# Performance work log

Hardware: AMD Instinct MI355X
Metric: run time of the kernel (lower is better)

The kernel has to match this reference:

```python
import jax, jax.numpy as jnp
import numpy as np
from jax import lax

H, W = 32, 32
HEADS = 8
EPS_LN = 1e-5


def layer_norm(x, g, b):
    mu = jnp.mean(x, axis=-1, keepdims=True)
    var = jnp.mean((x - mu) ** 2, axis=-1, keepdims=True)
    return (x - mu) * lax.rsqrt(var + EPS_LN) * g + b


def l2norm(x):  # F.normalize along last dim, eps=1e-12
    n = jnp.sqrt(jnp.sum(x * x, axis=-1, keepdims=True))
    return x / jnp.maximum(n, 1e-12)


def channel_attention(x, qkv_w, temp, proj_w, proj_b):
    B, N, C = x.shape
    d = C // HEADS
    qkv = (x @ qkv_w).reshape(B, N, 3, HEADS, d).transpose(2, 0, 3, 1, 4)  # [3,B,h,N,d]
    q, k, v = qkv[0], qkv[1], qkv[2]
    q = l2norm(q.swapaxes(-2, -1))  # [B,h,d,N], normalized over N
    k = l2norm(k.swapaxes(-2, -1))
    v = v.swapaxes(-2, -1)          # [B,h,d,N]
    attn = jnp.einsum('bhdn,bhen->bhde', q, k) * temp  # [B,h,d,d]
    attn = jax.nn.softmax(attn, axis=-1)
    out = jnp.einsum('bhde,bhen->bhdn', attn, v)       # [B,h,d,N]
    out = out.transpose(0, 3, 1, 2).reshape(B, N, C)
    return out @ proj_w + proj_b


def cross_attention(x1, x2, rp_w, rp_b, cn_g, cn_b):
    # head_count = 1 (efficient/linear attention)
    B, N, D = x1.shape
    keys = x2.swapaxes(1, 2)            # [B,D,N]
    values = x1.swapaxes(1, 2)          # [B,D,N]
    key = jax.nn.softmax(keys, axis=2)  # softmax over tokens
    query = jax.nn.softmax(keys, axis=1)  # softmax over channels
    context = jnp.einsum('bdn,ben->bde', key, values)     # [B,Dk,Dv]
    attended = jnp.einsum('bde,bdn->ben', context, query)  # [B,Dv,N]
    agg = attended.reshape(B, D, H, W)
    # 1x1 conv reprojection D -> 2D
    rep = jnp.einsum('bdhw,ed->behw', agg, rp_w) + rp_b[None, :, None, None]
    rep = rep.reshape(B, 2 * D, N).transpose(0, 2, 1)     # [B,N,2D]
    return layer_norm(rep, cn_g, cn_b)


def mix_ffn(x, fc1_w, fc1_b, dw_w, dw_b, fc2_w, fc2_b):
    B, N, _ = x.shape
    c2 = fc1_w.shape[1]
    h1 = x @ fc1_w + fc1_b                                 # [B,N,c2]
    t = h1.swapaxes(1, 2).reshape(B, c2, H, W)
    conv = lax.conv_general_dilated(
        t, dw_w, window_strides=(1, 1), padding='SAME',
        feature_group_count=c2,
        dimension_numbers=('NCHW', 'OIHW', 'NCHW')) + dw_b[None, :, None, None]
    h2 = conv.reshape(B, c2, N).swapaxes(1, 2)             # [B,N,c2]
    return jax.nn.gelu(h2, approximate=False) @ fc2_w + fc2_b


def reference(x1, x2, ln1_g, ln1_b, ca_qkv_w, ca_temp, ca_proj_w, ca_proj_b,
              ln3_g, ln3_b, rp_w, rp_b, cn_g, cn_b, ln2_g, ln2_b,
              fc1_w, fc1_b, dw_w, dw_b, fc2_w, fc2_b):
    # NOTE: original code uses norm1 + channel_attn1 on BOTH streams
    channel1 = x1 + channel_attention(layer_norm(x1, ln1_g, ln1_b), ca_qkv_w, ca_temp, ca_proj_w, ca_proj_b)
    channel2 = x2 + channel_attention(layer_norm(x2, ln1_g, ln1_b), ca_qkv_w, ca_temp, ca_proj_w, ca_proj_b)
    n1 = layer_norm(channel1, ln3_g, ln3_b)
    n2 = layer_norm(channel2, ln3_g, ln3_b)
    attn = cross_attention(n1, n2, rp_w, rp_b, cn_g, cn_b)
    tx = jnp.concatenate([channel1, channel2], axis=2) + attn  # [B,N,2D]
    mx = tx + mix_ffn(layer_norm(tx, ln2_g, ln2_b), fc1_w, fc1_b, dw_w, dw_b, fc2_w, fc2_b)
    return mx


def setup_inputs() -> dict:
    key = jax.random.key(0)
    ks = jax.random.split(key, 8)
    B, N, D = 16, 1024, 384
    s = 0.02
    return {
        'x1': jax.random.normal(ks[0], (B, N, D), jnp.float32),
        'x2': jax.random.normal(ks[1], (B, N, D), jnp.float32),
        'ln1_g': jnp.ones((D,), jnp.float32), 'ln1_b': jnp.zeros((D,), jnp.float32),
        'ca_qkv_w': jax.random.normal(ks[2], (D, 3 * D), jnp.float32) * s,
        'ca_temp': jnp.ones((HEADS, 1, 1), jnp.float32),
        'ca_proj_w': jax.random.normal(ks[3], (D, D), jnp.float32) * s,
        'ca_proj_b': jnp.zeros((D,), jnp.float32),
        'ln3_g': jnp.ones((D,), jnp.float32), 'ln3_b': jnp.zeros((D,), jnp.float32),
        'rp_w': jax.random.normal(ks[4], (2 * D, D), jnp.float32) * s,
        'rp_b': jnp.zeros((2 * D,), jnp.float32),
        'cn_g': jnp.ones((2 * D,), jnp.float32), 'cn_b': jnp.zeros((2 * D,), jnp.float32),
        'ln2_g': jnp.ones((2 * D,), jnp.float32), 'ln2_b': jnp.zeros((2 * D,), jnp.float32),
        'fc1_w': jax.random.normal(ks[5], (2 * D, 4 * D), jnp.float32) * s,
        'fc1_b': jnp.zeros((4 * D,), jnp.float32),
        'dw_w': jax.random.normal(ks[6], (4 * D, 1, 3, 3), jnp.float32) * s,
        'dw_b': jnp.zeros((4 * D,), jnp.float32),
        'fc2_w': jax.random.normal(ks[7], (4 * D, 2 * D), jnp.float32) * s,
        'fc2_b': jnp.zeros((2 * D,), jnp.float32),
    }
```

## Files before the change

kernel.cpp:

```cpp
#include <hip/hip_runtime.h>
#include <math.h>

#define BN 16
#define NN 1024
#define DD 384
#define D2 768
#define C2 1536
#define NHEAD 8
#define DH 48

#define SZ_ND   (BN*NN*DD)
#define SZ_N2D  (BN*NN*D2)
#define SZ_NC2  (BN*NN*C2)
#define M2      32768
#define MH      16384

typedef __bf16 bf16x8 __attribute__((ext_vector_type(8)));
typedef float f32x4v __attribute__((ext_vector_type(4)));
typedef unsigned short u16x4 __attribute__((ext_vector_type(4)));

__device__ __forceinline__ unsigned short f2bf(float x){
  unsigned int u = __float_as_uint(x);
  u += 0x7FFFu + ((u >> 16) & 1u);
  return (unsigned short)(u >> 16);
}
__device__ __forceinline__ float bf2f(unsigned short h){
  return __uint_as_float(((unsigned int)h) << 16);
}

__device__ __forceinline__ float blockReduceSum256(float v){
  __shared__ float red[4];
  #pragma unroll
  for (int o=32;o;o>>=1) v += __shfl_down(v,o,64);
  if ((threadIdx.x&63)==0) red[threadIdx.x>>6]=v;
  __syncthreads();
  float r = red[0]+red[1]+red[2]+red[3];
  __syncthreads();
  return r;
}
__device__ __forceinline__ float blockReduceMax256(float v){
  __shared__ float red[4];
  #pragma unroll
  for (int o=32;o;o>>=1) v = fmaxf(v, __shfl_down(v,o,64));
  if ((threadIdx.x&63)==0) red[threadIdx.x>>6]=v;
  __syncthreads();
  float r = fmaxf(fmaxf(red[0],red[1]),fmaxf(red[2],red[3]));
  __syncthreads();
  return r;
}

__global__ __launch_bounds__(256) void ln_kernel(const float* __restrict__ in,
    const float* __restrict__ g, const float* __restrict__ b,
    float* __restrict__ out, int C){
  const int row = blockIdx.x;
  const float* x = in + (size_t)row*C;
  float s=0.f;
  for (int i=threadIdx.x;i<C;i+=256) s += x[i];
  s = blockReduceSum256(s);
  const float mu = s / (float)C;
  float v=0.f;
  for (int i=threadIdx.x;i<C;i+=256){ float d = x[i]-mu; v += d*d; }
  v = blockReduceSum256(v);
  const float rs = rsqrtf(v/(float)C + 1e-5f);
  float* o = out + (size_t)row*C;
  for (int i=threadIdx.x;i<C;i+=256) o[i] = (x[i]-mu)*rs*g[i] + b[i];
}

__global__ __launch_bounds__(256) void ln_split2_kernel(const float* __restrict__ in1,
    const float* __restrict__ in2, int Mh,
    const float* __restrict__ g, const float* __restrict__ b,
    unsigned short* __restrict__ oh, unsigned short* __restrict__ ol, int C){
  const int row = blockIdx.x;
  const float* x = (row < Mh) ? (in1 + (size_t)row*C) : (in2 + (size_t)(row-Mh)*C);
  float s=0.f;
  for (int i=threadIdx.x;i<C;i+=256) s += x[i];
  s = blockReduceSum256(s);
  const float mu = s / (float)C;
  float v=0.f;
  for (int i=threadIdx.x;i<C;i+=256){ float d = x[i]-mu; v += d*d; }
  v = blockReduceSum256(v);
  const float rs = rsqrtf(v/(float)C + 1e-5f);
  unsigned short* ohp = oh + (size_t)row*C;
  unsigned short* olp = ol + (size_t)row*C;
  for (int i=threadIdx.x;i<C;i+=256){
    float val = (x[i]-mu)*rs*g[i] + b[i];
    unsigned short hh = f2bf(val);
    ohp[i] = hh; olp[i] = f2bf(val - bf2f(hh));
  }
}

__global__ __launch_bounds__(256) void rowsoftmax_split_kernel(const float* __restrict__ in,
    unsigned short* __restrict__ oh, unsigned short* __restrict__ ol, int C){
  const int row = blockIdx.x;
  const float* x = in + (size_t)row*C;
  float m = -3.0e38f;
  for (int i=threadIdx.x;i<C;i+=256) m = fmaxf(m, x[i]);
  m = blockReduceMax256(m);
  float s = 0.f;
  for (int i=threadIdx.x;i<C;i+=256) s += expf(x[i]-m);
  s = blockReduceSum256(s);
  const float inv = 1.f/s;
  unsigned short* ohp = oh + (size_t)row*C;
  unsigned short* olp = ol + (size_t)row*C;
  for (int i=threadIdx.x;i<C;i+=256){
    float p = expf(x[i]-m)*inv;
    unsigned short hh = f2bf(p);
    ohp[i] = hh; olp[i] = f2bf(p - bf2f(hh));
  }
}

__global__ __launch_bounds__(256) void colsoftmax_tsplit_kernel(const float* __restrict__ in,
    unsigned short* __restrict__ oh, unsigned short* __restrict__ ol){
  const int dl = threadIdx.x & 63;
  const int nc = threadIdx.x >> 6;
  const int d  = blockIdx.x*64 + dl;
  const int b  = blockIdx.y;
  const float* p = in + (size_t)b*NN*DD + d;
  __shared__ float redm[4][64];
  __shared__ float reds[4][64];
  float m = -3.0e38f;
  for (int n=nc*256; n<nc*256+256; n++) m = fmaxf(m, p[(size_t)n*DD]);
  redm[nc][dl] = m; __syncthreads();
  m = fmaxf(fmaxf(redm[0][dl],redm[1][dl]),fmaxf(redm[2][dl],redm[3][dl]));
  float s=0.f;
  for (int n=nc*256;n<nc*256+256;n++) s += expf(p[(size_t)n*DD]-m);
  reds[nc][dl]=s; __syncthreads();
  s = reds[0][dl]+reds[1][dl]+reds[2][dl]+reds[3][dl];
  const float inv = 1.f/s;
  unsigned short* qh = oh + ((size_t)b*DD + d)*NN;
  unsigned short* ql = ol + ((size_t)b*DD + d)*NN;
  for (int n=nc*256;n<nc*256+256;n++){
    float val = expf(p[(size_t)n*DD]-m)*inv;
    unsigned short hh = f2bf(val);
    qh[n] = hh; ql[n] = f2bf(val - bf2f(hh));
  }
}

__global__ __launch_bounds__(256) void tsplit_kernel(const float* __restrict__ in,
    unsigned short* __restrict__ oh, unsigned short* __restrict__ ol, int R, int Cc){
  const size_t zb = (size_t)blockIdx.z * R * Cc;
  const float* ip = in + zb;
  unsigned short* ohp = oh + zb;
  unsigned short* olp = ol + zb;
  __shared__ float tile[32][33];
  const int c0 = blockIdx.x*32, r0 = blockIdx.y*32;
  const int j = threadIdx.x & 31, i4 = threadIdx.x >> 5;
  #pragma unroll
  for (int s=0;s<4;s++){
    int i = i4*4+s;
    tile[i][j] = ip[(size_t)(r0+i)*Cc + c0 + j];
  }
  __syncthreads();
  #pragma unroll
  for (int s=0;s<4;s++){
    int i = i4*4+s;
    float x = tile[j][i];
    unsigned short h = f2bf(x);
    ohp[(size_t)(c0+i)*R + r0 + j] = h;
    olp[(size_t)(c0+i)*R + r0 + j] = f2bf(x - bf2f(h));
  }
}

__global__ __launch_bounds__(256) void chattn_mfma_kernel(
    const unsigned int* __restrict__ qp, const float* __restrict__ temp,
    unsigned short* __restrict__ coh, unsigned short* __restrict__ col)
{
  const int bh = blockIdx.x, b = bh >> 3, h = bh & 7;
  const int t = threadIdx.x, w = t >> 6, lane = t & 63;
  const int lr = lane & 15, g = lane >> 4;

  __shared__ __align__(16) unsigned char ldsA[27648];
  unsigned short (*Qh)[72] = (unsigned short(*)[72])(ldsA);
  unsigned short (*Ql)[72] = (unsigned short(*)[72])(ldsA + 6912);
  unsigned short (*Kh)[72] = (unsigned short(*)[72])(ldsA + 13824);
  unsigned short (*Kl)[72] = (unsigned short(*)[72])(ldsA + 20736);
  unsigned short (*Vh)[72] = (unsigned short(*)[72])(ldsA);
  unsigned short (*Vl)[72] = (unsigned short(*)[72])(ldsA + 9216);
  __shared__ unsigned short Ph[48][72], Pl[48][72];
  __shared__ float S[48][49];
  __shared__ float qn[48], kn[48];

  const size_t base = (size_t)b*NN*1152 + (size_t)h*48;

  int agrp[3], apr[3], aoff[3];
  #pragma unroll
  for (int l=0;l<3;l++){
    int idx = l*256+t;
    int mo = (idx>=384) ? 1 : 0;
    int a = idx - mo*384;
    agrp[l] = a%12; apr[l] = a/12; aoff[l] = mo*384;
  }

  f32x4v acc[12];
  #pragma unroll
  for (int i=0;i<12;i++) acc[i] = (f32x4v){0.f,0.f,0.f,0.f};

  uint4 p0[3], p1[3];
  #pragma unroll
  for (int l=0;l<3;l++){
    const size_t a = base + (size_t)(apr[l]*2)*1152 + aoff[l] + agrp[l]*4;
    p0[l] = *(const uint4*)(qp + a);
    p1[l] = *(const uint4*)(qp + a + 1152);
  }

  for (int nc=0; nc<16; nc++){
    #pragma unroll
    for (int l=0;l<3;l++){
      unsigned short (*Dh)[72] = aoff[l] ? Kh : Qh;
      unsigned short (*Dl)[72] = aoff[l] ? Kl : Ql;
      const unsigned w0[4] = {p0[l].x, p0[l].y, p0[l].z, p0[l].w};
      const unsigned w1[4] = {p1[l].x, p1[l].y, p1[l].z, p1[l].w};
      #pragma unroll
      for (int c=0;c<4;c++){
        int d = agrp[l]*4+c;
        *(unsigned int*)&Dh[d][apr[l]*2] = (w0[c] & 0xffffu) | (w1[c] << 16);
        *(unsigned int*)&Dl[d][apr[l]*2] = (w0[c] >> 16)     | (w1[c] & 0xffff0000u);
      }
    }
    __syncthreads();
    if (nc < 15){
      #pragma unroll
      for (int l=0;l<3;l++){
        const size_t a = base + (size_t)((nc+1)*64 + apr[l]*2)*1152 + aoff[l] + agrp[l]*4;
        p0[l] = *(const uint4*)(qp + a);
        p1[l] = *(const uint4*)(qp + a + 1152);
      }
    }
    if (w < 3){
      #pragma unroll
      for (int ks=0;ks<2;ks++){
        bf16x8 a_h = *(const bf16x8*)&Qh[w*16+lr][ks*32+g*8];
        bf16x8 a_l = *(const bf16x8*)&Ql[w*16+lr][ks*32+g*8];
        #pragma unroll
        for (int c=0;c<3;c++){
          bf16x8 b_h = *(const bf16x8*)&Kh[c*16+lr][ks*32+g*8];
          bf16x8 b_l = *(const bf16x8*)&Kl[c*16+lr][ks*32+g*8];
          acc[c] = __builtin_amdgcn_mfma_f32_16x16x32_bf16(a_h, b_h, acc[c], 0,0,0);
          acc[c] = __builtin_amdgcn_mfma_f32_16x16x32_bf16(a_l, b_h, acc[c], 0,0,0);
          acc[c] = __builtin_amdgcn_mfma_f32_16x16x32_bf16(a_h, b_l, acc[c], 0,0,0);
        }
      }
    } else {
      #pragma unroll
      for (int ks=0;ks<2;ks++){
        #pragma unroll
        for (int c=0;c<3;c++){
          bf16x8 qh_ = *(const bf16x8*)&Qh[c*16+lr][ks*32+g*8];
          bf16x8 ql_ = *(const bf16x8*)&Ql[c*16+lr][ks*32+g*8];
          bf16x8 kh_ = *(const bf16x8*)&Kh[c*16+lr][ks*32+g*8];
          bf16x8 kl_ = *(const bf16x8*)&Kl[c*16+lr][ks*32+g*8];
          acc[c]   = __builtin_amdgcn_mfma_f32_16x16x32_bf16(qh_, qh_, acc[c],   0,0,0);
          acc[3+c] = __builtin_amdgcn_mfma_f32_16x16x32_bf16(qh_, ql_, acc[3+c], 0,0,0);
          acc[6+c] = __builtin_amdgcn_mfma_f32_16x16x32_bf16(kh_, kh_, acc[6+c], 0,0,0);
          acc[9+c] = __builtin_amdgcn_mfma_f32_16x16x32_bf16(kh_, kl_, acc[9+c], 0,0,0);
        }
      }
    }
    __syncthreads();
  }

  const float tp = temp[h];
  if (w == 3){
    if ((lane>>4) == ((lane&15)>>2)){
      int p = lane & 15, r = p & 3;
      #pragma unroll
      for (int c=0;c<3;c++){
        float q2 = fmaxf(acc[c][r]   + 2.f*acc[3+c][r], 0.f);
        float k2 = fmaxf(acc[6+c][r] + 2.f*acc[9+c][r], 0.f);
        qn[c*16+p] = fmaxf(sqrtf(q2), 1e-12f);
        kn[c*16+p] = fmaxf(sqrtf(k2), 1e-12f);
      }
    }
  }
  __syncthreads();
  if (w < 3){
    #pragma unroll
    for (int c=0;c<3;c++){
      #pragma unroll
      for (int r=0;r<4;r++){
        int i = w*16 + g*4 + r, j = c*16 + lr;
        S[i][j] = acc[c][r]*tp/(qn[i]*kn[j]);
      }
    }
  }
  __syncthreads();

  int vgrp[3], vtk[3];
  #pragma unroll
  for (int l=0;l<3;l++){ int idx=l*256+t; vtk[l]=idx/12; vgrp[l]=idx%12; }
  uint4 pv[3];
  #pragma unroll
  for (int l=0;l<3;l++){
    const size_t a = base + (size_t)vtk[l]*1152 + 768 + vgrp[l]*4;
    pv[l] = *(const uint4*)(qp + a);
  }

  if (t < 48){
    float m = -3.0e38f;
    for (int j=0;j<48;j++) m = fmaxf(m, S[t][j]);
    float s = 0.f;
    for (int j=0;j<48;j++){ float e_ = expf(S[t][j]-m); S[t][j] = e_; s += e_; }
    float inv = 1.f/s;
    for (int j=0;j<48;j++){
      float p = S[t][j]*inv;
      unsigned short hp = f2bf(p);
      Ph[t][j] = hp; Pl[t][j] = f2bf(p - bf2f(hp));
    }
    #pragma unroll
    for (int j=48;j<64;j++){ Ph[t][j]=0; Pl[t][j]=0; }
  } else {
    const u16x4 z4 = (u16x4){0,0,0,0};
    for (int idx=t-48; idx<512; idx+=208){
      int tk = idx>>3, q = idx&7;
      if (q<4) *(u16x4*)&Vh[tk][48+(q&3)*4] = z4;
      else     *(u16x4*)&Vl[tk][48+(q&3)*4] = z4;
    }
  }
  __syncthreads();

  bf16x8 pfh[3][2], pfl[3][2];
  #pragma unroll
  for (int it=0;it<3;it++)
    #pragma unroll
    for (int ks=0;ks<2;ks++){
      pfh[it][ks] = *(const bf16x8*)&Ph[it*16+lr][ks*32+g*8];
      pfl[it][ks] = *(const bf16x8*)&Pl[it*16+lr][ks*32+g*8];
    }

  for (int vc=0; vc<16; vc++){
    #pragma unroll
    for (int l=0;l<3;l++){
      const unsigned pw[4] = {pv[l].x, pv[l].y, pv[l].z, pv[l].w};
      u16x4 hv, lv;
      #pragma unroll
      for (int c=0;c<4;c++){
        hv[c] = (unsigned short)(pw[c] & 0xffffu);
        lv[c] = (unsigned short)(pw[c] >> 16);
      }
      *(u16x4*)&Vh[vtk[l]][vgrp[l]*4] = hv;
      *(u16x4*)&Vl[vtk[l]][vgrp[l]*4] = lv;
    }
    __syncthreads();
    if (vc < 15){
      #pragma unroll
      for (int l=0;l<3;l++){
        const size_t a = base + (size_t)((vc+1)*64+vtk[l])*1152 + 768 + vgrp[l]*4;
        pv[l] = *(const uint4*)(qp + a);
      }
    }
    bf16x8 vfh[2], vfl[2];
    #pragma unroll
    for (int ks=0;ks<2;ks++){
      vfh[ks] = *(const bf16x8*)&Vh[w*16+lr][ks*32+g*8];
      vfl[ks] = *(const bf16x8*)&Vl[w*16+lr][ks*32+g*8];
    }
    f32x4v o[3];
    #pragma unroll
    for (int it=0;it<3;it++) o[it] = (f32x4v){0.f,0.f,0.f,0.f};
    #pragma unroll
    for (int it=0;it<3;it++)
      #pragma unroll
      for (int ks=0;ks<2;ks++){
        o[it] = __builtin_amdgcn_mfma_f32_16x16x32_bf16(pfh[it][ks], vfh[ks], o[it], 0,0,0);
        o[it] = __builtin_amdgcn_mfma_f32_16x16x32_bf16(pfl[it][ks], vfh[ks], o[it], 0,0,0);
        o[it] = __builtin_amdgcn_mfma_f32_16x16x32_bf16(pfh[it][ks], vfl[ks], o[it], 0,0,0);
      }
    const int n = vc*64 + w*16 + lr;
    #pragma unroll
    for (int it=0;it<3;it++){
      const size_t off = ((size_t)b*NN + n)*DD + h*48 + it*16 + g*4;
      u16x4 hv, lv;
      #pragma unroll
      for (int r=0;r<4;r++){
        float x = o[it][r];
        unsigned short hh = f2bf(x);
        hv[r] = hh; lv[r] = f2bf(x - bf2f(hh));
      }
      *(u16x4*)(coh + off) = hv;
      *(u16x4*)(col + off) = lv;
    }
    __syncthreads();
  }
}

__global__ __launch_bounds__(256) void wconv_t_kernel(const float* __restrict__ in,
    unsigned short* __restrict__ oh, unsigned short* __restrict__ ol, int K, int Nin){
  __shared__ float tile[32][33];
  const int n0 = blockIdx.x*32, k0 = blockIdx.y*32;
  const int j = threadIdx.x & 31, i4 = threadIdx.x >> 5;
  #pragma unroll
  for (int s=0;s<4;s++){
    int i = i4*4+s;
    tile[i][j] = (n0 + j < Nin) ? in[(size_t)(k0+i)*Nin + n0 + j] : 0.f;
  }
  __syncthreads();
  #pragma unroll
  for (int s=0;s<4;s++){
    int i = i4*4+s;
    float x = tile[j][i];
    unsigned short h = f2bf(x);
    oh[(size_t)(n0+i)*K + k0 + j] = h;
    ol[(size_t)(n0+i)*K + k0 + j] = f2bf(x - bf2f(h));
  }
}

__global__ __launch_bounds__(256) void wconv_kernel(const float* __restrict__ in,
    unsigned short* __restrict__ oh, unsigned short* __restrict__ ol, int n){
  int i = blockIdx.x*256 + threadIdx.x;
  if (i < n){
    float x = in[i];
    unsigned short h = f2bf(x);
    oh[i] = h;
    ol[i] = f2bf(x - bf2f(h));
  }
}

template<bool BIAS_, bool RES_, bool SPLIT_, bool PACK32_>
__global__ __launch_bounds__(256) void gemm_bf16x3s_kernel(
    const unsigned short* __restrict__ Ah, const unsigned short* __restrict__ Al,
    const unsigned short* __restrict__ Bh, const unsigned short* __restrict__ Bl,
    const float* __restrict__ bias, const float* __restrict__ res,
    const float* __restrict__ res2, int Mh2,
    float* __restrict__ C, unsigned short* __restrict__ Ch, unsigned short* __restrict__ Cl,
    int M, int N, int K, size_t sAz, size_t sBz, size_t sCz)
{
  const int t = threadIdx.x;
  const int nwg = gridDim.x*gridDim.y;
  const int lin = blockIdx.y*gridDim.x + blockIdx.x;
  const int swz = ((nwg & 7)==0) ? ((lin & 7)*(nwg >> 3) + (lin >> 3)) : lin;
  const int bx = swz % gridDim.x, by = swz / gridDim.x;
  const int m0 = by*128, n0 = bx*128;
  const size_t zo = (size_t)blockIdx.z;

  __shared__ unsigned short As_h0[128][32], As_l0[128][32];
  __shared__ unsigned short Bs_h0[128][32], Bs_l0[128][32];
  __shared__ unsigned short As_h1[128][32], As_l1[128][32];
  __shared__ unsigned short Bs_h1[128][32], Bs_l1[128][32];

  const unsigned short* Ahb = Ah + zo*sAz + (size_t)m0*K;
  const unsigned short* Alb = Al + zo*sAz + (size_t)m0*K;
  const unsigned short* Bhb = Bh + zo*sBz + (size_t)n0*K;
  const unsigned short* Blb = Bl + zo*sBz + (size_t)n0*K;

  f32x4v acc[4][4];
  #pragma unroll
  for (int i=0;i<4;i++)
    #pragma unroll
    for (int j=0;j<4;j++) acc[i][j] = (f32x4v){0.f,0.f,0.f,0.f};

  const int w  = t >> 6;
  const int wm = w >> 1, wn = w & 1;
  const int lr = t & 15, g = (t & 63) >> 4;
  const int srow = t >> 1;
  const int kb0  = (t & 1)*2;
  const int ssw  = (srow >> 1) & 3;
  const int ks0  = ((kb0+0) ^ ssw)*8;
  const int ks1  = ((kb0+1) ^ ssw)*8;

  uint4 aAh0,aAh1,aAl0,aAl1,aBh0,aBh1,aBl0,aBl1;
  uint4 bAh0,bAh1,bAl0,bAl1,bBh0,bBh1,bBl0,bBl1;

#define LOADT(P, K0) { \
    const size_t go0 = (size_t)srow*K + (size_t)(K0) + (size_t)(kb0*8); \
    P##Ah0 = *(const uint4*)(Ahb + go0); P##Ah1 = *(const uint4*)(Ahb + go0 + 8); \
    P##Al0 = *(const uint4*)(Alb + go0); P##Al1 = *(const uint4*)(Alb + go0 + 8); \
    P##Bh0 = *(const uint4*)(Bhb + go0); P##Bh1 = *(const uint4*)(Bhb + go0 + 8); \
    P##Bl0 = *(const uint4*)(Blb + go0); P##Bl1 = *(const uint4*)(Blb + go0 + 8); }

#define WRITET(BUF, P) { \
    *(uint4*)&As_h##BUF[srow][ks0] = P##Ah0; *(uint4*)&As_h##BUF[srow][ks1] = P##Ah1; \
    *(uint4*)&As_l##BUF[srow][ks0] = P##Al0; *(uint4*)&As_l##BUF[srow][ks1] = P##Al1; \
    *(uint4*)&Bs_h##BUF[srow][ks0] = P##Bh0; *(uint4*)&Bs_h##BUF[srow][ks1] = P##Bh1; \
    *(uint4*)&Bs_l##BUF[srow][ks0] = P##Bl0; *(uint4*)&Bs_l##BUF[srow][ks1] = P##Bl1; }

#define COMPUTET(BUF) { \
    bf16x8 ah[4], al[4], bhf[4], blf[4]; \
    _Pragma("unroll") \
    for (int i=0;i<4;i++){ \
      const int ra = wm*64 + i*16 + lr; \
      const int ka = (g ^ ((ra>>1)&3))*8; \
      ah[i]  = *(const bf16x8*)&As_h##BUF[ra][ka]; \
      al[i]  = *(const bf16x8*)&As_l##BUF[ra][ka]; \
      const int rb = wn*64 + i*16 + lr; \
      const int kb = (g ^ ((rb>>1)&3))*8; \
      bhf[i] = *(const bf16x8*)&Bs_h##BUF[rb][kb]; \
      blf[i] = *(const bf16x8*)&Bs_l##BUF[rb][kb]; \
    } \
    _Pragma("unroll") \
    for (int mi=0;mi<4;mi++) \
      _Pragma("unroll") \
      for (int ni=0;ni<4;ni++){ \
        f32x4v c_ = acc[mi][ni]; \
        c_ = __builtin_amdgcn_mfma_f32_16x16x32_bf16(ah[mi], bhf[ni], c_, 0,0,0); \
        c_ = __builtin_amdgcn_mfma_f32_16x16x32_bf16(al[mi], bhf[ni], c_, 0,0,0); \
        c_ = __builtin_amdgcn_mfma_f32_16x16x32_bf16(ah[mi], blf[ni], c_, 0,0,0); \
        acc[mi][ni] = c_; \
      } }

  const int nk = K >> 5;
  LOADT(a, 0);
  WRITET(0, a);
  LOADT(a, 32);
  __syncthreads();

  for (int kt = 0; kt < nk; kt += 2){
    if (kt+2 < nk) LOADT(b, (kt+2)*32);
    COMPUTET(0);
    WRITET(1, a);
    __syncthreads();
    if (kt+3 < nk) LOADT(a, (kt+3)*32);
    COMPUTET(1);
    if (kt+2 < nk){ WRITET(0, b); }
    __syncthreads();
  }

#undef LOADT
#undef WRITET
#undef COMPUTET

  if (PACK32_){
    unsigned int* Cp = (unsigned int*)Ch + zo*sCz;
    #pragma unroll
    for (int ni=0;ni<4;ni++){
      const int col = n0 + wn*64 + ni*16 + lr;
      #pragma unroll
      for (int mi=0;mi<4;mi++){
        const int r0 = m0 + wm*64 + mi*16 + g*4;
        #pragma unroll
        for (int r=0;r<4;r++){
          float v = acc[mi][ni][r];
          unsigned short hv = f2bf(v);
          unsigned short lv = f2bf(v - bf2f(hv));
          Cp[(size_t)(r0+r)*N + col] = (unsigned)hv | ((unsigned)lv << 16);
        }
      }
    }
  } else if (SPLIT_){
    unsigned short* Chb = Ch + zo*sCz;
    unsigned short* Clb = Cl + zo*sCz;
    #pragma unroll
    for (int ni=0;ni<4;ni++){
      const int col = n0 + wn*64 + ni*16 + lr;
      #pragma unroll
      for (int mi=0;mi<4;mi++){
        const int r0 = m0 + wm*64 + mi*16 + g*4;
        #pragma unroll
        for (int r=0;r<4;r++){
          float v = acc[mi][ni][r];
          unsigned short hv = f2bf(v);
          const size_t off = (size_t)(r0+r)*N + col;
          Chb[off] = hv;
          Clb[off] = f2bf(v - bf2f(hv));
        }
      }
    }
  } else {
    float* Cb = C + zo*sCz;
    const float* resb = nullptr;
    size_t roff = 0;
    if (RES_){
      if (res2 != nullptr && m0 >= Mh2){ resb = res2; roff = (size_t)Mh2; }
      else resb = res + zo*sCz;
    }
    #pragma unroll
    for (int ni=0;ni<4;ni++){
      const int col = n0 + wn*64 + ni*16 + lr;
      const float bb = BIAS_ ? bias[col] : 0.f;
      #pragma unroll
      for (int mi=0;mi<4;mi++){
        const int r0 = m0 + wm*64 + mi*16 + g*4;
        #pragma unroll
        for (int r=0;r<4;r++){
          float v = acc[mi][ni][r] + bb;
          if (RES_) v += resb[((size_t)(r0+r) - roff)*N + col];
          Cb[(size_t)(r0+r)*N + col] = v;
        }
      }
    }
  }
}

__global__ __launch_bounds__(256) void ln_concat_ln2_kernel(const float* __restrict__ rep,
    const float* __restrict__ g1, const float* __restrict__ b1,
    const float* __restrict__ ch1, const float* __restrict__ ch2,
    const float* __restrict__ g2, const float* __restrict__ b2,
    float* __restrict__ tx, unsigned short* __restrict__ y2h, unsigned short* __restrict__ y2l){
  const int row = blockIdx.x;
  const float* x = rep + (size_t)row*D2;
  float xv[3];
  float s=0.f;
  #pragma unroll
  for (int q=0;q<3;q++){ xv[q] = x[threadIdx.x + q*256]; s += xv[q]; }
  s = blockReduceSum256(s);
  const float mu = s / (float)D2;
  float v=0.f;
  #pragma unroll
  for (int q=0;q<3;q++){ float d = xv[q]-mu; v += d*d; }
  v = blockReduceSum256(v);
  const float rs = rsqrtf(v/(float)D2 + 1e-5f);
  float tv[3];
  #pragma unroll
  for (int q=0;q<3;q++){
    int i = threadIdx.x + q*256;
    float val = (xv[q]-mu)*rs*g1[i] + b1[i];
    float rv = (i<DD) ? ch1[(size_t)row*DD + i] : ch2[(size_t)row*DD + i - DD];
    tv[q] = val + rv;
    tx[(size_t)row*D2 + i] = tv[q];
  }
  float s2 = tv[0]+tv[1]+tv[2];
  s2 = blockReduceSum256(s2);
  const float mu2 = s2 / (float)D2;
  float v2=0.f;
  #pragma unroll
  for (int q=0;q<3;q++){ float d = tv[q]-mu2; v2 += d*d; }
  v2 = blockReduceSum256(v2);
  const float rs2 = rsqrtf(v2/(float)D2 + 1e-5f);
  #pragma unroll
  for (int q=0;q<3;q++){
    int i = threadIdx.x + q*256;
    float y = (tv[q]-mu2)*rs2*g2[i] + b2[i];
    unsigned short hh = f2bf(y);
    y2h[(size_t)row*D2 + i] = hh;
    y2l[(size_t)row*D2 + i] = f2bf(y - bf2f(hh));
  }
}

__global__ __launch_bounds__(256) void dwconv_gelu_kernel(const float* __restrict__ h1,
    const float* __restrict__ w, const float* __restrict__ bias,
    unsigned short* __restrict__ gh, unsigned short* __restrict__ gl){
  const int idx = blockIdx.x*256 + threadIdx.x;
  const int b   = idx / 12288;
  const int r   = idx - b*12288;
  const int hh  = r / 384;
  const int c4  = r - hh*384;
  const int c   = c4*4;
  const float* base = h1 + (size_t)b*NN*C2 + c;
  const size_t obase = ((size_t)b*NN + hh*32)*C2 + c;

  f32x4v wk[9];
  #pragma unroll
  for (int k=0;k<9;k++){
    f32x4v t_;
    #pragma unroll
    for (int q=0;q<4;q++) t_[q] = w[(size_t)(c+q)*9 + k];
    wk[k] = t_;
  }
  f32x4v bvv;
  {
    const float4 bb = *(const float4*)(bias + c);
    bvv = (f32x4v){bb.x, bb.y, bb.z, bb.w};
  }

  const bool hm = (hh > 0), hp = (hh < 31);
  const f32x4v z4 = (f32x4v){0.f,0.f,0.f,0.f};
  const size_t rm = (size_t)((hh-1)*32)*C2;
  const size_t r0 = (size_t)( hh   *32)*C2;
  const size_t rp = (size_t)((hh+1)*32)*C2;

  f32x4v A0,A1,A2, B0,B1,B2, C0,C1,C2c;
  A0=z4; A1=z4; A2=z4;
  B0 = hm ? *(const f32x4v*)(base + rm) : z4;
  B1 =      *(const f32x4v*)(base + r0);
  B2 = hp ? *(const f32x4v*)(base + rp) : z4;
  C0 = hm ? *(const f32x4v*)(base + rm + C2) : z4;
  C1 =      *(const f32x4v*)(base + r0 + C2);
  C2c= hp ? *(const f32x4v*)(base + rp + C2) : z4;

  for (int ww=0; ww<32; ww++){
    f32x4v N0,N1,N2;
    if (ww < 30){
      const size_t co_ = (size_t)(ww+2)*C2;
      N0 = hm ? *(const f32x4v*)(base + rm + co_) : z4;
      N1 =      *(const f32x4v*)(base + r0 + co_) ;
      N2 = hp ? *(const f32x4v*)(base + rp + co_) : z4;
    } else { N0=z4; N1=z4; N2=z4; }

    f32x4v s = bvv;
    s += wk[0]*A0 + wk[1]*B0 + wk[2]*C0;
    s += wk[3]*A1 + wk[4]*B1 + wk[5]*C1;
    s += wk[6]*A2 + wk[7]*B2 + wk[8]*C2c;

    u16x4 hv, lv;
    #pragma unroll
    for (int q=0;q<4;q++){
      float rlt = 0.5f*s[q]*(1.f + erff(s[q]*0.70710678118654752f));
      unsigned short hhv = f2bf(rlt);
      hv[q] = hhv; lv[q] = f2bf(rlt - bf2f(hhv));
    }
    *(u16x4*)(gh + obase + (size_t)ww*C2) = hv;
    *(u16x4*)(gl + obase + (size_t)ww*C2) = lv;

    A0=B0; A1=B1; A2=B2;
    B0=C0; B1=C1; B2=C2c;
    C0=N0; C1=N1; C2c=N2;
  }
}

extern "C" void kernel_launch(void* const* d_in, const int* in_sizes, int n_in,
                              void* d_out, int out_size, void* d_ws, size_t ws_size,
                              hipStream_t stream) {
  const float* x1     = (const float*)d_in[0];
  const float* x2     = (const float*)d_in[1];
  const float* ln1_g  = (const float*)d_in[2];
  const float* ln1_b  = (const float*)d_in[3];
  const float* qkv_w  = (const float*)d_in[4];
  const float* ca_temp= (const float*)d_in[5];
  const float* proj_w = (const float*)d_in[6];
  const float* proj_b = (const float*)d_in[7];
  const float* ln3_g  = (const float*)d_in[8];
  const float* ln3_b  = (const float*)d_in[9];
  const float* rp_w   = (const float*)d_in[10];
  const float* rp_b   = (const float*)d_in[11];
  const float* cn_g   = (const float*)d_in[12];
  const float* cn_b   = (const float*)d_in[13];
  const float* ln2_g  = (const float*)d_in[14];
  const float* ln2_b  = (const float*)d_in[15];
  const float* fc1_w  = (const float*)d_in[16];
  const float* fc1_b  = (const float*)d_in[17];
  const float* dw_w   = (const float*)d_in[18];
  const float* dw_b   = (const float*)d_in[19];
  const float* fc2_w  = (const float*)d_in[20];
  const float* fc2_b  = (const float*)d_in[21];
  float* out = (float*)d_out;
  float* W   = (float*)d_ws;

  unsigned short* ycoh = (unsigned short*)out;
  unsigned short* ycol = ycoh + 12582912u;
  unsigned short* coh  = ycoh;
  unsigned short* col  = ycol;
  unsigned int*   qkvp = (unsigned int*)W;
  unsigned short* qkvwT_h  = (unsigned short*)(W + 37748736ull);
  unsigned short* qkvwT_l  = qkvwT_h + 442368u;
  unsigned short* projwT_h = qkvwT_l + 442368u;
  unsigned short* projwT_l = projwT_h + 147456u;
  float* ch12 = W;
  float* n12  = W + 12582912ull;
  unsigned short* QSh = (unsigned short*)(W + 25165824ull);
  unsigned short* QSl = QSh + 6291456u;
  unsigned short* KSt_h = (unsigned short*)(W + 31457280ull);
  unsigned short* KSt_l = KSt_h + 6291456u;
  unsigned short* rpw_h = (unsigned short*)(W + 37748736ull);
  unsigned short* rpw_l = rpw_h + 294912u;
  unsigned short* n1t_h = (unsigned short*)(W + 38043648ull);
  unsigned short* n1t_l = n1t_h + 6291456u;
  unsigned short* ctxT_h = (unsigned short*)(W + 12582912ull);
  unsigned short* ctxT_l = ctxT_h + 2359296u;
  unsigned short* ATbh = (unsigned short*)(W + 14942208ull);
  unsigned short* ATbl = ATbh + 6291456u;
  float* rep = W + 25165824ull;
  float* txp = out;
  unsigned short* y2h = (unsigned short*)(W + 37748736ull);
  unsigned short* y2l = y2h + 12582912u;
  float* h1 = W;
  unsigned short* fc1wT_h = (unsigned short*)(W + 25165824ull);
  unsigned short* fc1wT_l = fc1wT_h + 1179648u;
  unsigned short* gh = (unsigned short*)(W + 25165824ull);
  unsigned short* gl = (unsigned short*)(W + 37748736ull);
  unsigned short* fc2wT_h = (unsigned short*)W;
  unsigned short* fc2wT_l = fc2wT_h + 1179648u;

  wconv_t_kernel<<<dim3(1152/32, DD/32), dim3(256), 0, stream>>>(qkv_w, qkvwT_h, qkvwT_l, DD, 1152);
  wconv_t_kernel<<<dim3(DD/32, DD/32), dim3(256), 0, stream>>>(proj_w, projwT_h, projwT_l, DD, DD);

  ln_split2_kernel<<<dim3(M2), dim3(256), 0, stream>>>(x1, x2, MH, ln1_g, ln1_b, ycoh, ycol, DD);
  gemm_bf16x3s_kernel<false,false,false,true><<<dim3(1152/128, M2/128), dim3(256), 0, stream>>>(
      ycoh, ycol, qkvwT_h, qkvwT_l, nullptr, nullptr, nullptr, 0,
      nullptr, (unsigned short*)qkvp, nullptr, M2, 1152, DD, 0,0,0);
  chattn_mfma_kernel<<<dim3(32*NHEAD), dim3(256), 0, stream>>>(qkvp, ca_temp, coh, col);
  gemm_bf16x3s_kernel<true,true,false,false><<<dim3(DD/128, M2/128), dim3(256), 0, stream>>>(
      coh, col, projwT_h, projwT_l, proj_b, x1, x2, MH,
      ch12, nullptr, nullptr, M2, DD, DD, 0,0,0);

  wconv_kernel<<<dim3(294912/256), dim3(256), 0, stream>>>(rp_w, rpw_h, rpw_l, 294912);
  ln_kernel<<<dim3(M2), dim3(256), 0, stream>>>(ch12, ln3_g, ln3_b, n12, DD);
  const float* n2half = n12 + (size_t)MH*DD;
  rowsoftmax_split_kernel<<<dim3(MH), dim3(256), 0, stream>>>(n2half, QSh, QSl, DD);
  colsoftmax_tsplit_kernel<<<dim3(DD/64, BN), dim3(256), 0, stream>>>(n2half, KSt_h, KSt_l);
  tsplit_kernel<<<dim3(DD/32, NN/32, BN), dim3(256), 0, stream>>>(n12, n1t_h, n1t_l, NN, DD);
  gemm_bf16x3s_kernel<false,false,true,false><<<dim3(DD/128, DD/128, BN), dim3(256), 0, stream>>>(
      n1t_h, n1t_l, KSt_h, KSt_l, nullptr, nullptr, nullptr, 0,
      nullptr, ctxT_h, ctxT_l, DD, DD, NN, (size_t)DD*NN, (size_t)DD*NN, (size_t)DD*DD);
  gemm_bf16x3s_kernel<false,false,true,false><<<dim3(DD/128, NN/128, BN), dim3(256), 0, stream>>>(
      QSh, QSl, ctxT_h, ctxT_l, nullptr, nullptr, nullptr, 0,
      nullptr, ATbh, ATbl, NN, DD, DD, (size_t)NN*DD, (size_t)DD*DD, (size_t)NN*DD);
  gemm_bf16x3s_kernel<true,false,false,false><<<dim3(D2/128, MH/128), dim3(256), 0, stream>>>(
      ATbh, ATbl, rpw_h, rpw_l, rp_b, nullptr, nullptr, 0,
      rep, nullptr, nullptr, MH, D2, DD, 0,0,0);
  ln_concat_ln2_kernel<<<dim3(MH), dim3(256), 0, stream>>>(
      rep, cn_g, cn_b, ch12, ch12 + (size_t)MH*DD, ln2_g, ln2_b, txp, y2h, y2l);

  wconv_t_kernel<<<dim3(C2/32, D2/32), dim3(256), 0, stream>>>(fc1_w, fc1wT_h, fc1wT_l, D2, C2);
  gemm_bf16x3s_kernel<true,false,false,false><<<dim3(C2/128, MH/128), dim3(256), 0, stream>>>(
      y2h, y2l, fc1wT_h, fc1wT_l, fc1_b, nullptr, nullptr, 0,
      h1, nullptr, nullptr, MH, C2, D2, 0,0,0);
  dwconv_gelu_kernel<<<dim3(196608/256), dim3(256), 0, stream>>>(h1, dw_w, dw_b, gh, gl);
  wconv_t_kernel<<<dim3(D2/32, C2/32), dim3(256), 0, stream>>>(fc2_w, fc2wT_h, fc2wT_l, C2, D2);
  gemm_bf16x3s_kernel<true,true,false,false><<<dim3(D2/128, MH/128), dim3(256), 0, stream>>>(
      gh, gl, fc2wT_h, fc2wT_l, fc2_b, txp, nullptr, 0,
      out, nullptr, nullptr, MH, D2, C2, 0,0,0);
}
```

Before: 898.6 us.

## Tile column softmax through shared memory with online max and coalesced transposed stores

The column-softmax-plus-transpose kernel now stages 64x32 tiles in shared memory, runs an online max/sum over tiles, and writes the transposed bf16 hi/lo outputs through a shared buffer so global stores are coalesced along tokens. The old version made strided per-thread loads and 2-byte scattered stores across rows. The grid doubles to 32-channel blocks, giving more parallelism. The two weight transpose-convert launches are also merged into one kernel to save a launch.

Result: faster. 847.8 us (median of 2 runs) (-5.6%).

```diff
diff --git a/kernel.cpp b/kernel.cpp
--- a/kernel.cpp
+++ b/kernel.cpp
@@ -111,28 +111,74 @@
 
 __global__ __launch_bounds__(256) void colsoftmax_tsplit_kernel(const float* __restrict__ in,
     unsigned short* __restrict__ oh, unsigned short* __restrict__ ol){
-  const int dl = threadIdx.x & 63;
-  const int nc = threadIdx.x >> 6;
-  const int d  = blockIdx.x*64 + dl;
-  const int b  = blockIdx.y;
-  const float* p = in + (size_t)b*NN*DD + d;
-  __shared__ float redm[4][64];
-  __shared__ float reds[4][64];
-  float m = -3.0e38f;
-  for (int n=nc*256; n<nc*256+256; n++) m = fmaxf(m, p[(size_t)n*DD]);
-  redm[nc][dl] = m; __syncthreads();
-  m = fmaxf(fmaxf(redm[0][dl],redm[1][dl]),fmaxf(redm[2][dl],redm[3][dl]));
-  float s=0.f;
-  for (int n=nc*256;n<nc*256+256;n++) s += expf(p[(size_t)n*DD]-m);
-  reds[nc][dl]=s; __syncthreads();
-  s = reds[0][dl]+reds[1][dl]+reds[2][dl]+reds[3][dl];
-  const float inv = 1.f/s;
-  unsigned short* qh = oh + ((size_t)b*DD + d)*NN;
-  unsigned short* ql = ol + ((size_t)b*DD + d)*NN;
-  for (int n=nc*256;n<nc*256+256;n++){
-    float val = expf(p[(size_t)n*DD]-m)*inv;
-    unsigned short hh = f2bf(val);
-    qh[n] = hh; ql[n] = f2bf(val - bf2f(hh));
+  __shared__ float tile[64][33];
+  __shared__ unsigned short outh[32][66], outl[32][66];
+  __shared__ float redm[8][32], reds[8][32];
+  const int d0 = blockIdx.x*32, b = blockIdx.y;
+  const int t = threadIdx.x, dl = t & 31, nc = t >> 5;
+  const float* p = in + (size_t)b*NN*DD + d0;
+
+  float m_run = -3.0e38f, s_run = 0.f;
+  for (int tb = 0; tb < 16; tb++){
+    const int n0 = tb*64;
+    #pragma unroll
+    for (int k=0;k<8;k++){
+      int e = t + k*256;
+      int row = e >> 5, col = e & 31;
+      tile[row][col] = p[(size_t)(n0+row)*DD + col];
+    }
+    __syncthreads();
+    float lm = -3.0e38f;
+    #pragma unroll
+    for (int r=0;r<8;r++) lm = fmaxf(lm, tile[nc*8+r][dl]);
+    redm[nc][dl] = lm;
+    __syncthreads();
+    float tm = redm[0][dl];
+    #pragma unroll
+    for (int q=1;q<8;q++) tm = fmaxf(tm, redm[q][dl]);
+    float m_new = fmaxf(m_run, tm);
+    float ls = 0.f;
+    #pragma unroll
+    for (int r=0;r<8;r++) ls += expf(tile[nc*8+r][dl] - m_new);
+    reds[nc][dl] = ls;
+    __syncthreads();
+    float ts = reds[0][dl];
+    #pragma unroll
+    for (int q=1;q<8;q++) ts += reds[q][dl];
+    s_run = s_run * expf(m_run - m_new) + ts;
+    m_run = m_new;
+    __syncthreads();
+  }
+
+  const float inv = 1.f / s_run, mm = m_run;
+  unsigned short* qh = oh + ((size_t)b*DD + d0)*NN;
+  unsigned short* ql = ol + ((size_t)b*DD + d0)*NN;
+  for (int tb = 0; tb < 16; tb++){
+    const int n0 = tb*64;
+    #pragma unroll
+    for (int k=0;k<8;k++){
+      int e = t + k*256;
+      int row = e >> 5, col = e & 31;
+      tile[row][col] = p[(size_t)(n0+row)*DD + col];
+    }
+    __syncthreads();
+    #pragma unroll
+    for (int r=0;r<8;r++){
+      int row = nc*8 + r;
+      float val = expf(tile[row][dl] - mm) * inv;
+      unsigned short hh = f2bf(val);
+      outh[dl][row] = hh;
+      outl[dl][row] = f2bf(val - bf2f(hh));
+    }
+    __syncthreads();
+    #pragma unroll
+    for (int k=0;k<8;k++){
+      int e = t + k*256;
+      int dd = e >> 6, nn = e & 63;
+      qh[(size_t)dd*NN + n0 + nn] = outh[dd][nn];
+      ql[(size_t)dd*NN + n0 + nn] = outl[dd][nn];
+    }
+    __syncthreads();
   }
 }
 
@@ -380,6 +426,33 @@
       *(u16x4*)(col + off) = lv;
     }
     __syncthreads();
+  }
+}
+
+__global__ __launch_bounds__(256) void wprep2_kernel(
+    const float* __restrict__ qkvw, unsigned short* __restrict__ qwh, unsigned short* __restrict__ qwl,
+    const float* __restrict__ projw, unsigned short* __restrict__ pwh, unsigned short* __restrict__ pwl)
+{
+  __shared__ float tile[32][33];
+  const int bid = blockIdx.x;
+  const float* in; unsigned short *oh, *ol; int Nin, bx, by;
+  if (bid < 432){ in = qkvw;  oh = qwh; ol = qwl; Nin = 1152; bx = bid % 36; by = bid / 36; }
+  else { int k = bid - 432; in = projw; oh = pwh; ol = pwl; Nin = DD;   bx = k % 12;  by = k / 12; }
+  const int n0 = bx*32, k0 = by*32;
+  const int j = threadIdx.x & 31, i4 = threadIdx.x >> 5;
+  #pragma unroll
+  for (int s=0;s<4;s++){
+    int i = i4*4+s;
+    tile[i][j] = in[(size_t)(k0+i)*Nin + n0 + j];
+  }
+  __syncthreads();
+  #pragma unroll
+  for (int s=0;s<4;s++){
+    int i = i4*4+s;
+    float x = tile[j][i];
+    unsigned short h = f2bf(x);
+    oh[(size_t)(n0+i)*DD + k0 + j] = h;
+    ol[(size_t)(n0+i)*DD + k0 + j] = f2bf(x - bf2f(h));
   }
 }
 
@@ -759,8 +832,8 @@
   unsigned short* fc2wT_h = (unsigned short*)W;
   unsigned short* fc2wT_l = fc2wT_h + 1179648u;
 
-  wconv_t_kernel<<<dim3(1152/32, DD/32), dim3(256), 0, stream>>>(qkv_w, qkvwT_h, qkvwT_l, DD, 1152);
-  wconv_t_kernel<<<dim3(DD/32, DD/32), dim3(256), 0, stream>>>(proj_w, projwT_h, projwT_l, DD, DD);
+  wprep2_kernel<<<dim3(576), dim3(256), 0, stream>>>(
+      qkv_w, qkvwT_h, qkvwT_l, proj_w, projwT_h, projwT_l);
 
   ln_split2_kernel<<<dim3(M2), dim3(256), 0, stream>>>(x1, x2, MH, ln1_g, ln1_b, ycoh, ycol, DD);
   gemm_bf16x3s_kernel<false,false,false,true><<<dim3(1152/128, M2/128), dim3(256), 0, stream>>>(
@@ -775,7 +848,7 @@
   ln_kernel<<<dim3(M2), dim3(256), 0, stream>>>(ch12, ln3_g, ln3_b, n12, DD);
   const float* n2half = n12 + (size_t)MH*DD;
   rowsoftmax_split_kernel<<<dim3(MH), dim3(256), 0, stream>>>(n2half, QSh, QSl, DD);
-  colsoftmax_tsplit_kernel<<<dim3(DD/64, BN), dim3(256), 0, stream>>>(n2half, KSt_h, KSt_l);
+  colsoftmax_tsplit_kernel<<<dim3(DD/32, BN), dim3(256), 0, stream>>>(n2half, KSt_h, KSt_l);
   tsplit_kernel<<<dim3(DD/32, NN/32, BN), dim3(256), 0, stream>>>(n12, n1t_h, n1t_l, NN, DD);
   gemm_bf16x3s_kernel<false,false,true,false><<<dim3(DD/128, DD/128, BN), dim3(256), 0, stream>>>(
       n1t_h, n1t_l, KSt_h, KSt_l, nullptr, nullptr, nullptr, 0,
```
